# Performance work log

Measured on AMD Instinct MI355X. Metric: run time of the kernel, lower is better.

Reference implementation:

```python
import jax, jax.numpy as jnp
import numpy as np

S, B, D, H, DH, E, F = 2048, 2, 512, 8, 64, 8, 1024
TOPK = 2


def setup_inputs() -> dict:
    key = jax.random.key(0)
    ks = jax.random.split(key, 12)
    rn = lambda k, shp, s=0.02: jax.random.normal(k, shp, jnp.float32) * s
    # RoPE tables (half-split convention): (S, DH)
    pos = jnp.arange(S, dtype=jnp.float32)[:, None]
    inv_freq = 1.0 / (10000.0 ** (jnp.arange(0, DH, 2, dtype=jnp.float32) / DH))
    ang = pos * inv_freq[None, :]                       # (S, DH//2)
    cos = jnp.concatenate([jnp.cos(ang), jnp.cos(ang)], axis=-1)
    sin = jnp.concatenate([jnp.sin(ang), jnp.sin(ang)], axis=-1)
    return {
        "src": jax.random.normal(ks[0], (S, B, D), jnp.float32),
        "cos": cos, "sin": sin,
        "Wq": rn(ks[1], (D, D)), "bq": jnp.zeros((D,), jnp.float32),
        "Wk": rn(ks[2], (D, D)), "bk": jnp.zeros((D,), jnp.float32),
        "Wv": rn(ks[3], (D, D)), "bv": jnp.zeros((D,), jnp.float32),
        "Wo": rn(ks[4], (D, D)), "bo": jnp.zeros((D,), jnp.float32),
        "ln1_g": jnp.ones((D,), jnp.float32), "ln1_b": jnp.zeros((D,), jnp.float32),
        "ln2_g": jnp.ones((D,), jnp.float32), "ln2_b": jnp.zeros((D,), jnp.float32),
        "Wg": rn(ks[5], (D, E)),
        "W1": rn(ks[6], (E, D, F)), "B1": jnp.zeros((E, F), jnp.float32),
        "W2": rn(ks[7], (E, F, D)), "B2": jnp.zeros((E, D), jnp.float32),
    }


def _layernorm(x, g, b, eps=1e-5):
    m = x.mean(-1, keepdims=True)
    v = ((x - m) ** 2).mean(-1, keepdims=True)
    return (x - m) * jax.lax.rsqrt(v + eps) * g + b


def _rotate_half(x):
    x1, x2 = jnp.split(x, 2, axis=-1)
    return jnp.concatenate([-x2, x1], axis=-1)


def _forward(src, cos, sin, Wq, bq, Wk, bk, Wv, bv, Wo, bo,
             ln1_g, ln1_b, ln2_g, ln2_b, Wg, W1, B1, W2, B2):
    # ---- RoPE self-attention ----
    q = (src @ Wq + bq).reshape(S, B, H, DH)
    k = (src @ Wk + bk).reshape(S, B, H, DH)
    v = (src @ Wv + bv).reshape(S, B, H, DH)
    c = cos[:, None, None, :]
    s = sin[:, None, None, :]
    q = q * c + _rotate_half(q) * s
    k = k * c + _rotate_half(k) * s
    scores = jnp.einsum("sbhd,tbhd->bhst", q, k) / jnp.sqrt(jnp.float32(DH))
    attn = jax.nn.softmax(scores, axis=-1)              # (B,H,S,S)
    ctx = jnp.einsum("bhst,tbhd->sbhd", attn, v).reshape(S, B, D)
    attn_out = ctx @ Wo + bo
    x = _layernorm(src + attn_out, ln1_g, ln1_b)
    # ---- MoE feed-forward (top-k softmax gating) ----
    xt = x.reshape(S * B, D)                            # (N, D)
    probs = jax.nn.softmax(xt @ Wg, axis=-1)            # (N, E)
    top_v, top_i = jax.lax.top_k(probs, TOPK)           # (N, TOPK)
    top_v = top_v / top_v.sum(-1, keepdims=True)
    N = S * B
    gates = jnp.zeros((N, E), jnp.float32).at[
        jnp.arange(N)[:, None], top_i].add(top_v)       # (N, E)
    h = jax.nn.relu(jnp.einsum("nd,edf->nef", xt, W1) + B1[None])   # (N,E,F)
    eo = jnp.einsum("nef,efd->ned", h, W2) + B2[None]               # (N,E,D)
    moe_out = jnp.einsum("ne,ned->nd", gates, eo).reshape(S, B, D)
    return _layernorm(x + moe_out, ln2_g, ln2_b)


def reference(src, cos, sin, Wq, bq, Wk, bk, Wv, bv, Wo, bo,
              ln1_g, ln1_b, ln2_g, ln2_b, Wg, W1, B1, W2, B2):
    return _forward(src, cos, sin, Wq, bq, Wk, bk, Wv, bv, Wo, bo,
                    ln1_g, ln1_b, ln2_g, ln2_b, Wg, W1, B1, W2, B2)
```

## Files before the change

### kernel.cpp

```cpp
#include <hip/hip_runtime.h>
#include <math.h>

#define S_  2048
#define B_  2
#define D_  512
#define H_  8
#define DH_ 64
#define E_  8
#define F_  1024
#define N_  4096
#define NPAIR_ 8192

typedef __attribute__((ext_vector_type(4))) float f32x4;
typedef __attribute__((ext_vector_type(8))) short short8;
typedef unsigned short u16;

__device__ __forceinline__ u16 f2bf(float f) {
  unsigned u = __builtin_bit_cast(unsigned, f);
  u += 0x7fffu + ((u >> 16) & 1u);
  return (u16)(u >> 16);
}
__device__ __forceinline__ float bf2f(u16 h) {
  unsigned u = ((unsigned)h) << 16;
  return __builtin_bit_cast(float, u);
}

__global__ __launch_bounds__(256) void src_split(const float* __restrict__ in,
                                                 u16* __restrict__ hi,
                                                 u16* __restrict__ lo) {
  size_t i = ((size_t)blockIdx.x * 256 + threadIdx.x) * 8;
  float f[8];
  *(float4*)&f[0] = *(const float4*)&in[i];
  *(float4*)&f[4] = *(const float4*)&in[i + 4];
  short8 h, l;
#pragma unroll
  for (int j = 0; j < 8; ++j) {
    u16 a = f2bf(f[j]);
    h[j] = (short)a;
    l[j] = (short)f2bf(f[j] - bf2f(a));
  }
  *(short8*)&hi[i] = h;
  *(short8*)&lo[i] = l;
}

__global__ __launch_bounds__(256) void wsplit_t(const float* __restrict__ W,
                                                u16* __restrict__ Whi,
                                                u16* __restrict__ Wlo,
                                                int Nn, int K) {
  __shared__ u16 Th[64][72];
  __shared__ u16 Tl[64][72];
  int kb = blockIdx.y * 64, nb = blockIdx.x * 64;
  int r = threadIdx.x >> 2, c0 = (threadIdx.x & 3) * 16;
  const float* wp = &W[(size_t)(kb + r) * Nn + nb + c0];
#pragma unroll
  for (int c = 0; c < 16; c += 4) {
    float4 t = *(const float4*)&wp[c];
    float f[4] = {t.x, t.y, t.z, t.w};
#pragma unroll
    for (int j = 0; j < 4; ++j) {
      u16 a = f2bf(f[j]);
      Th[r][c0 + c + j] = a;
      Tl[r][c0 + c + j] = f2bf(f[j] - bf2f(a));
    }
  }
  __syncthreads();
  short8 h0, h1, l0, l1;
#pragma unroll
  for (int j = 0; j < 8; ++j) {
    h0[j] = (short)Th[c0 + j][r];     h1[j] = (short)Th[c0 + 8 + j][r];
    l0[j] = (short)Tl[c0 + j][r];     l1[j] = (short)Tl[c0 + 8 + j][r];
  }
  size_t ob = (size_t)(nb + r) * K + kb + c0;
  *(short8*)&Whi[ob] = h0;  *(short8*)&Whi[ob + 8] = h1;
  *(short8*)&Wlo[ob] = l0;  *(short8*)&Wlo[ob + 8] = l1;
}

__global__ __launch_bounds__(256) void wtrans(const float* __restrict__ W,
                                              u16* __restrict__ Wt,
                                              int K, int Nn) {
  size_t eo = (size_t)blockIdx.z * K * Nn;
  __shared__ u16 T[64][72];
  int kb = blockIdx.y * 64, nb = blockIdx.x * 64;
  int r = threadIdx.x >> 2, c0 = (threadIdx.x & 3) * 16;
  const float* wp = &W[eo + (size_t)(kb + r) * Nn + nb + c0];
#pragma unroll
  for (int c = 0; c < 16; c += 4) {
    float4 t = *(const float4*)&wp[c];
    T[r][c0 + c + 0] = f2bf(t.x);
    T[r][c0 + c + 1] = f2bf(t.y);
    T[r][c0 + c + 2] = f2bf(t.z);
    T[r][c0 + c + 3] = f2bf(t.w);
  }
  __syncthreads();
  short8 s0, s1;
#pragma unroll
  for (int j = 0; j < 8; ++j) {
    s0[j] = (short)T[c0 + j][r];
    s1[j] = (short)T[c0 + 8 + j][r];
  }
  *(short8*)&Wt[eo + (size_t)(nb + r) * K + kb + c0] = s0;
  *(short8*)&Wt[eo + (size_t)(nb + r) * K + kb + c0 + 8] = s1;
}

__global__ __launch_bounds__(256) void qkv_mfma(const u16* __restrict__ Ah_g,
                                                const u16* __restrict__ Al_g,
                                                const u16* __restrict__ Bh_g,
                                                const u16* __restrict__ Bl_g,
                                                const float* __restrict__ bq,
                                                const float* __restrict__ bk,
                                                const float* __restrict__ bv,
                                                const float* __restrict__ cosb,
                                                const float* __restrict__ sinb,
                                                u16* __restrict__ qh, u16* __restrict__ ql,
                                                u16* __restrict__ kh, u16* __restrict__ kl,
                                                u16* __restrict__ vb) {
  __shared__ u16 Ah[128][40], Al[128][40], Bh[128][40], Bl[128][40];
  int tid = threadIdx.x;
  int w = tid >> 6, l = tid & 63;
  int wr = w >> 1, wc = w & 1;
  int lg = l >> 4, lx = l & 15;
  int m0 = blockIdx.x * 128, n0 = blockIdx.y * 128;
  int sr = tid >> 1, s16 = (tid & 1) * 16;
  const u16* Aph = Ah_g + (size_t)(m0 + sr) * 512;
  const u16* Apl = Al_g + (size_t)(m0 + sr) * 512;
  const u16* Bph = Bh_g + (size_t)(n0 + sr) * 512;
  const u16* Bpl = Bl_g + (size_t)(n0 + sr) * 512;
  f32x4 acc[4][4];
#pragma unroll
  for (int m = 0; m < 4; ++m)
#pragma unroll
    for (int n = 0; n < 4; ++n) acc[m][n] = (f32x4){0.f, 0.f, 0.f, 0.f};
  short8 ah0 = *(const short8*)&Aph[s16];
  short8 ah1 = *(const short8*)&Aph[s16 + 8];
  short8 al0 = *(const short8*)&Apl[s16];
  short8 al1 = *(const short8*)&Apl[s16 + 8];
  short8 bh0 = *(const short8*)&Bph[s16];
  short8 bh1 = *(const short8*)&Bph[s16 + 8];
  short8 bl0 = *(const short8*)&Bpl[s16];
  short8 bl1 = *(const short8*)&Bpl[s16 + 8];
  for (int k0 = 0; k0 < 512; k0 += 32) {
    __syncthreads();
    *(short8*)&Ah[sr][s16] = ah0; *(short8*)&Ah[sr][s16 + 8] = ah1;
    *(short8*)&Al[sr][s16] = al0; *(short8*)&Al[sr][s16 + 8] = al1;
    *(short8*)&Bh[sr][s16] = bh0; *(short8*)&Bh[sr][s16 + 8] = bh1;
    *(short8*)&Bl[sr][s16] = bl0; *(short8*)&Bl[sr][s16 + 8] = bl1;
    __syncthreads();
    if (k0 + 32 < 512) {
      int ko = k0 + 32 + s16;
      ah0 = *(const short8*)&Aph[ko]; ah1 = *(const short8*)&Aph[ko + 8];
      al0 = *(const short8*)&Apl[ko]; al1 = *(const short8*)&Apl[ko + 8];
      bh0 = *(const short8*)&Bph[ko]; bh1 = *(const short8*)&Bph[ko + 8];
      bl0 = *(const short8*)&Bpl[ko]; bl1 = *(const short8*)&Bpl[ko + 8];
    }
    short8 fah[4], fal[4], fbh[4], fbl[4];
#pragma unroll
    for (int m = 0; m < 4; ++m) {
      fah[m] = *(const short8*)&Ah[wr * 64 + m * 16 + lx][lg * 8];
      fal[m] = *(const short8*)&Al[wr * 64 + m * 16 + lx][lg * 8];
    }
#pragma unroll
    for (int n = 0; n < 4; ++n) {
      fbh[n] = *(const short8*)&Bh[wc * 64 + n * 16 + lx][lg * 8];
      fbl[n] = *(const short8*)&Bl[wc * 64 + n * 16 + lx][lg * 8];
    }
#pragma unroll
    for (int m = 0; m < 4; ++m)
#pragma unroll
      for (int n = 0; n < 4; ++n) {
        acc[m][n] = __builtin_amdgcn_mfma_f32_16x16x32_bf16(fah[m], fbh[n], acc[m][n], 0, 0, 0);
        acc[m][n] = __builtin_amdgcn_mfma_f32_16x16x32_bf16(fal[m], fbh[n], acc[m][n], 0, 0, 0);
        acc[m][n] = __builtin_amdgcn_mfma_f32_16x16x32_bf16(fah[m], fbl[n], acc[m][n], 0, 0, 0);
      }
  }
  int tcolbase = n0 + wc * 64;
  int tsel = tcolbase >> 9;
  int hbase = tcolbase & 511;
  const float* bias = (tsel == 0) ? bq : (tsel == 1) ? bk : bv;
  if (tsel == 2) {
#pragma unroll
    for (int m = 0; m < 4; ++m)
#pragma unroll
      for (int i = 0; i < 4; ++i) {
        int row = m0 + wr * 64 + m * 16 + lg * 4 + i;
#pragma unroll
        for (int n = 0; n < 4; ++n) {
          int col = hbase + n * 16 + lx;
          vb[(size_t)row * 512 + col] = f2bf(acc[m][n][i] + bias[col]);
        }
      }
  } else {
    u16* oh = tsel ? kh : qh;
    u16* ol = tsel ? kl : ql;
    float qsc = tsel ? 1.f : 0.125f;
#pragma unroll
    for (int m = 0; m < 4; ++m)
#pragma unroll
      for (int i = 0; i < 4; ++i) {
        int row = m0 + wr * 64 + m * 16 + lg * 4 + i;
        int s = row >> 1;
#pragma unroll
        for (int n = 0; n < 2; ++n) {
          int dln = n * 16 + lx;
          float c  = cosb[s * 64 + dln];
          float sn = sinb[s * 64 + dln];
          float a  = acc[m][n][i]     + bias[hbase + dln];
          float b2 = acc[m][n + 2][i] + bias[hbase + dln + 32];
          float ra = (a * c - b2 * sn) * qsc;
          float rb = (b2 * c + a * sn) * qsc;
          size_t ix = (size_t)row * 512 + hbase + dln;
          u16 rah = f2bf(ra);
          oh[ix] = rah; ol[ix] = f2bf(ra - bf2f(rah));
          u16 rbh = f2bf(rb);
          oh[ix + 32] = rbh; ol[ix + 32] = f2bf(rb - bf2f(rbh));
        }
      }
  }
}

__global__ __launch_bounds__(256) void attn_mfma2(const u16* __restrict__ qh,
                                                  const u16* __restrict__ ql,
                                                  const u16* __restrict__ kh,
                                                  const u16* __restrict__ kl,
                                                  const u16* __restrict__ vbuf,
                                                  u16* __restrict__ poh,
                                                  u16* __restrict__ pol,
                                                  float* __restrict__ pml) {
  __shared__ u16 Khi[64][72];
  __shared__ u16 Klo[64][72];
  __shared__ u16 Vt[64][72];
  __shared__ u16 Pl[4][16][72];
  int tid = threadIdx.x;
  int w = tid >> 6, l = tid & 63;
  int lg = l >> 4, lx = l & 15;
  int f = blockIdx.x;
  int xcd = f & 7, j = f >> 3;
  int slab = xcd + 8 * (j & 3);
  int qt = j >> 2;
  int bh = slab >> 1, kvh = slab & 1;
  int b = bh >> 3, h = bh & 7;

  short8 qfh[2], qfl[2];
  {
    int qrow = qt * 64 + w * 16 + lx;
    size_t qo = (size_t)(qrow * 2 + b) * 512 + h * 64 + lg * 8;
    qfh[0] = *(const short8*)&qh[qo];
    qfh[1] = *(const short8*)&qh[qo + 32];
    qfl[0] = *(const short8*)&ql[qo];
    qfl[1] = *(const short8*)&ql[qo + 32];
  }

  f32x4 o_acc[4];
#pragma unroll
  for (int dg = 0; dg < 4; ++dg) o_acc[dg] = (f32x4){0.f, 0.f, 0.f, 0.f};
  float m_run[4], l_run[4];
#pragma unroll
  for (int i = 0; i < 4; ++i) { m_run[i] = -1e30f; l_run[i] = 0.f; }

  int kvr = tid >> 2, ds4 = (tid & 3) * 16;
  int kvc = tid & 63, dsg = (tid >> 6) * 16;
  int psw = ((lx >> 2) & 3) << 3;

  short8 rkh0, rkh1, rkl0, rkl1, rv0, rv1;
  {
    int t0 = kvh * 1024;
    size_t ko = (size_t)((t0 + kvr) * 2 + b) * 512 + h * 64 + ds4;
    rkh0 = *(const short8*)&kh[ko]; rkh1 = *(const short8*)&kh[ko + 8];
    rkl0 = *(const short8*)&kl[ko]; rkl1 = *(const short8*)&kl[ko + 8];
    size_t vo = (size_t)((t0 + kvc) * 2 + b) * 512 + h * 64 + dsg;
    rv0 = *(const short8*)&vbuf[vo]; rv1 = *(const short8*)&vbuf[vo + 8];
  }

  for (int tt = 0; tt < 1024; tt += 64) {
    __syncthreads();
    *(short8*)&Khi[kvr][ds4]     = rkh0;
    *(short8*)&Khi[kvr][ds4 + 8] = rkh1;
    *(short8*)&Klo[kvr][ds4]     = rkl0;
    *(short8*)&Klo[kvr][ds4 + 8] = rkl1;
#pragma unroll
    for (int c = 0; c < 8; ++c) {
      Vt[dsg + c][kvc] = (u16)rv0[c];
      Vt[dsg + 8 + c][kvc] = (u16)rv1[c];
    }
    __syncthreads();
    if (tt + 64 < 1024) {
      int t0 = kvh * 1024 + tt + 64;
      size_t ko = (size_t)((t0 + kvr) * 2 + b) * 512 + h * 64 + ds4;
      rkh0 = *(const short8*)&kh[ko]; rkh1 = *(const short8*)&kh[ko + 8];
      rkl0 = *(const short8*)&kl[ko]; rkl1 = *(const short8*)&kl[ko + 8];
      size_t vo = (size_t)((t0 + kvc) * 2 + b) * 512 + h * 64 + dsg;
      rv0 = *(const short8*)&vbuf[vo]; rv1 = *(const short8*)&vbuf[vo + 8];
    }

    f32x4 sc[4];
#pragma unroll
    for (int cg = 0; cg < 4; ++cg) {
      short8 kf0 = *(const short8*)&Khi[cg * 16 + lx][lg * 8];
      short8 kf1 = *(const short8*)&Khi[cg * 16 + lx][32 + lg * 8];
      short8 kg0 = *(const short8*)&Klo[cg * 16 + lx][lg * 8];
      short8 kg1 = *(const short8*)&Klo[cg * 16 + lx][32 + lg * 8];
      f32x4 a = (f32x4){0.f, 0.f, 0.f, 0.f};
      a = __builtin_amdgcn_mfma_f32_16x16x32_bf16(qfh[0], kf0, a, 0, 0, 0);
      a = __builtin_amdgcn_mfma_f32_16x16x32_bf16(qfh[1], kf1, a, 0, 0, 0);
      a = __builtin_amdgcn_mfma_f32_16x16x32_bf16(qfl[0], kf0, a, 0, 0, 0);
      a = __builtin_amdgcn_mfma_f32_16x16x32_bf16(qfl[1], kf1, a, 0, 0, 0);
      a = __builtin_amdgcn_mfma_f32_16x16x32_bf16(qfh[0], kg0, a, 0, 0, 0);
      a = __builtin_amdgcn_mfma_f32_16x16x32_bf16(qfh[1], kg1, a, 0, 0, 0);
      sc[cg] = a;
    }

#pragma unroll
    for (int i = 0; i < 4; ++i) {
      float s0 = sc[0][i], s1 = sc[1][i], s2 = sc[2][i], s3 = sc[3][i];
      float tm = fmaxf(fmaxf(s0, s1), fmaxf(s2, s3));
      tm = fmaxf(tm, __shfl_xor(tm, 1));
      tm = fmaxf(tm, __shfl_xor(tm, 2));
      tm = fmaxf(tm, __shfl_xor(tm, 4));
      tm = fmaxf(tm, __shfl_xor(tm, 8));
      float mn = fmaxf(m_run[i], tm);
      float corr = __expf(m_run[i] - mn);
      m_run[i] = mn;
      float p0 = __expf(s0 - mn), p1 = __expf(s1 - mn);
      float p2 = __expf(s2 - mn), p3 = __expf(s3 - mn);
      float ts = p0 + p1 + p2 + p3;
      ts += __shfl_xor(ts, 1); ts += __shfl_xor(ts, 2);
      ts += __shfl_xor(ts, 4); ts += __shfl_xor(ts, 8);
      l_run[i] = l_run[i] * corr + ts;
#pragma unroll
      for (int dg = 0; dg < 4; ++dg) o_acc[dg][i] *= corr;
      int row = lg * 4 + i;
      int sw = ((row >> 2) & 3) << 3;
      Pl[w][row][lx ^ sw]        = f2bf(p0);
      Pl[w][row][(16 + lx) ^ sw] = f2bf(p1);
      Pl[w][row][(32 + lx) ^ sw] = f2bf(p2);
      Pl[w][row][(48 + lx) ^ sw] = f2bf(p3);
    }

    short8 pa0 = *(const short8*)&Pl[w][lx][(lg * 8) ^ psw];
    short8 pa1 = *(const short8*)&Pl[w][lx][(32 + lg * 8) ^ psw];
#pragma unroll
    for (int dg = 0; dg < 4; ++dg) {
      short8 v0 = *(const short8*)&Vt[dg * 16 + lx][lg * 8];
      short8 v1 = *(const short8*)&Vt[dg * 16 + lx][32 + lg * 8];
      o_acc[dg] = __builtin_amdgcn_mfma_f32_16x16x32_bf16(pa0, v0, o_acc[dg], 0, 0, 0);
      o_acc[dg] = __builtin_amdgcn_mfma_f32_16x16x32_bf16(pa1, v1, o_acc[dg], 0, 0, 0);
    }
  }

#pragma unroll
  for (int i = 0; i < 4; ++i) {
    int srow = qt * 64 + w * 16 + lg * 4 + i;
    int row2 = srow * 2 + b;
    size_t base = (size_t)kvh * ((size_t)N_ * D_) + (size_t)row2 * 512 + h * 64;
#pragma unroll
    for (int dg = 0; dg < 4; ++dg) {
      float val = o_acc[dg][i];
      u16 hi = f2bf(val);
      poh[base + dg * 16 + lx] = hi;
      pol[base + dg * 16 + lx] = f2bf(val - bf2f(hi));
    }
    if (lx == 0) {
      int u = row2 * 8 + h;
      pml[(size_t)kvh * 65536 + u * 2 + 0] = m_run[i];
      pml[(size_t)kvh * 65536 + u * 2 + 1] = l_run[i];
    }
  }
}

__global__ __launch_bounds__(256) void merge_attn2(const u16* __restrict__ poh,
                                                   const u16* __restrict__ pol,
                                                   const float* __restrict__ pml,
                                                   u16* __restrict__ ch,
                                                   u16* __restrict__ cl) {
  int u = blockIdx.x * 4 + (threadIdx.x >> 6);
  int lane = threadIdx.x & 63;
  float m0 = pml[u * 2], l0 = pml[u * 2 + 1];
  float m1 = pml[65536 + u * 2], l1 = pml[65536 + u * 2 + 1];
  float m = fmaxf(m0, m1);
  float e0 = __expf(m0 - m), e1 = __expf(m1 - m);
  float inv = 1.f / (l0 * e0 + l1 * e1);
  int n = u >> 3, h = u & 7;
  size_t base = (size_t)n * 512 + h * 64 + lane;
  const size_t PO1 = (size_t)N_ * D_;
  float v0 = bf2f(poh[base]) + bf2f(pol[base]);
  float v1 = bf2f(poh[PO1 + base]) + bf2f(pol[PO1 + base]);
  float val = (v0 * e0 + v1 * e1) * inv;
  u16 hi = f2bf(val);
  ch[base] = hi;
  cl[base] = f2bf(val - bf2f(hi));
}

__global__ __launch_bounds__(256) void wo_mfma(const u16* __restrict__ Ah_g,
                                               const u16* __restrict__ Al_g,
                                               const u16* __restrict__ Bh_g,
                                               const u16* __restrict__ Bl_g,
                                               const float* __restrict__ bias,
                                               float* __restrict__ C) {
  __shared__ u16 Ah[128][40], Al[128][40], Bh[128][40], Bl[128][40];
  int tid = threadIdx.x;
  int w = tid >> 6, l = tid & 63;
  int wr = w >> 1, wc = w & 1;
  int lg = l >> 4, lx = l & 15;
  int m0 = blockIdx.x * 128, n0 = blockIdx.y * 128;
  int sr = tid >> 1, s16 = (tid & 1) * 16;
  const u16* Aph = Ah_g + (size_t)(m0 + sr) * 512;
  const u16* Apl = Al_g + (size_t)(m0 + sr) * 512;
  const u16* Bph = Bh_g + (size_t)(n0 + sr) * 512;
  const u16* Bpl = Bl_g + (size_t)(n0 + sr) * 512;
  f32x4 acc[4][4];
#pragma unroll
  for (int m = 0; m < 4; ++m)
#pragma unroll
    for (int n = 0; n < 4; ++n) acc[m][n] = (f32x4){0.f, 0.f, 0.f, 0.f};
  short8 ah0 = *(const short8*)&Aph[s16];
  short8 ah1 = *(const short8*)&Aph[s16 + 8];
  short8 al0 = *(const short8*)&Apl[s16];
  short8 al1 = *(const short8*)&Apl[s16 + 8];
  short8 bh0 = *(const short8*)&Bph[s16];
  short8 bh1 = *(const short8*)&Bph[s16 + 8];
  short8 bl0 = *(const short8*)&Bpl[s16];
  short8 bl1 = *(const short8*)&Bpl[s16 + 8];
  for (int k0 = 0; k0 < 512; k0 += 32) {
    __syncthreads();
    *(short8*)&Ah[sr][s16] = ah0; *(short8*)&Ah[sr][s16 + 8] = ah1;
    *(short8*)&Al[sr][s16] = al0; *(short8*)&Al[sr][s16 + 8] = al1;
    *(short8*)&Bh[sr][s16] = bh0; *(short8*)&Bh[sr][s16 + 8] = bh1;
    *(short8*)&Bl[sr][s16] = bl0; *(short8*)&Bl[sr][s16 + 8] = bl1;
    __syncthreads();
    if (k0 + 32 < 512) {
      int ko = k0 + 32 + s16;
      ah0 = *(const short8*)&Aph[ko]; ah1 = *(const short8*)&Aph[ko + 8];
      al0 = *(const short8*)&Apl[ko]; al1 = *(const short8*)&Apl[ko + 8];
      bh0 = *(const short8*)&Bph[ko]; bh1 = *(const short8*)&Bph[ko + 8];
      bl0 = *(const short8*)&Bpl[ko]; bl1 = *(const short8*)&Bpl[ko + 8];
    }
    short8 fah[4], fal[4], fbh[4], fbl[4];
#pragma unroll
    for (int m = 0; m < 4; ++m) {
      fah[m] = *(const short8*)&Ah[wr * 64 + m * 16 + lx][lg * 8];
      fal[m] = *(const short8*)&Al[wr * 64 + m * 16 + lx][lg * 8];
    }
#pragma unroll
    for (int n = 0; n < 4; ++n) {
      fbh[n] = *(const short8*)&Bh[wc * 64 + n * 16 + lx][lg * 8];
      fbl[n] = *(const short8*)&Bl[wc * 64 + n * 16 + lx][lg * 8];
    }
#pragma unroll
    for (int m = 0; m < 4; ++m)
#pragma unroll
      for (int n = 0; n < 4; ++n) {
        acc[m][n] = __builtin_amdgcn_mfma_f32_16x16x32_bf16(fah[m], fbh[n], acc[m][n], 0, 0, 0);
        acc[m][n] = __builtin_amdgcn_mfma_f32_16x16x32_bf16(fal[m], fbh[n], acc[m][n], 0, 0, 0);
        acc[m][n] = __builtin_amdgcn_mfma_f32_16x16x32_bf16(fah[m], fbl[n], acc[m][n], 0, 0, 0);
      }
  }
#pragma unroll
  for (int m = 0; m < 4; ++m)
#pragma unroll
    for (int i = 0; i < 4; ++i) {
      int row = m0 + wr * 64 + m * 16 + lg * 4 + i;
#pragma unroll
      for (int n = 0; n < 4; ++n) {
        int col = n0 + wc * 64 + n * 16 + lx;
        C[(size_t)row * 512 + col] = acc[m][n][i] + bias[col];
      }
    }
}

__global__ __launch_bounds__(256) void ln_res(const float* __restrict__ a,
                                              const float* __restrict__ b,
                                              const float* __restrict__ g,
                                              const float* __restrict__ beta,
                                              float* __restrict__ out,
                                              u16* __restrict__ obf) {
  int n = blockIdx.x * 4 + (threadIdx.x >> 6);
  int lane = threadIdx.x & 63;
  float v[8];
  float s = 0.f;
#pragma unroll
  for (int i = 0; i < 8; ++i) {
    int d = lane + 64 * i;
    v[i] = a[(size_t)n * D_ + d] + b[(size_t)n * D_ + d];
    s += v[i];
  }
#pragma unroll
  for (int m = 32; m; m >>= 1) s += __shfl_xor(s, m);
  float mean = s * (1.f / D_);
  float s2 = 0.f;
#pragma unroll
  for (int i = 0; i < 8; ++i) { float t = v[i] - mean; s2 += t * t; }
#pragma unroll
  for (int m = 32; m; m >>= 1) s2 += __shfl_xor(s2, m);
  float r = rsqrtf(s2 * (1.f / D_) + 1e-5f);
#pragma unroll
  for (int i = 0; i < 8; ++i) {
    int d = lane + 64 * i;
    float val = (v[i] - mean) * r * g[d] + beta[d];
    out[(size_t)n * D_ + d] = val;
    obf[(size_t)n * D_ + d] = f2bf(val);
  }
}

__global__ __launch_bounds__(256) void ln2_final(const float* __restrict__ x,
                                                 const u16* __restrict__ mp,
                                                 const float* __restrict__ g,
                                                 const float* __restrict__ beta,
                                                 float* __restrict__ out) {
  int n = blockIdx.x * 4 + (threadIdx.x >> 6);
  int lane = threadIdx.x & 63;
  float v[8];
  float s = 0.f;
#pragma unroll
  for (int i = 0; i < 8; ++i) {
    int d = lane + 64 * i;
    v[i] = x[(size_t)n * D_ + d] + bf2f(mp[(size_t)(2 * n) * D_ + d]) +
           bf2f(mp[(size_t)(2 * n + 1) * D_ + d]);
    s += v[i];
  }
#pragma unroll
  for (int m = 32; m; m >>= 1) s += __shfl_xor(s, m);
  float mean = s * (1.f / D_);
  float s2 = 0.f;
#pragma unroll
  for (int i = 0; i < 8; ++i) { float t = v[i] - mean; s2 += t * t; }
#pragma unroll
  for (int m = 32; m; m >>= 1) s2 += __shfl_xor(s2, m);
  float r = rsqrtf(s2 * (1.f / D_) + 1e-5f);
#pragma unroll
  for (int i = 0; i < 8; ++i) {
    int d = lane + 64 * i;
    out[(size_t)n * D_ + d] = (v[i] - mean) * r * g[d] + beta[d];
  }
}

__global__ __launch_bounds__(256) void gate_compute(const float* __restrict__ x,
                                                    const float* __restrict__ Wg,
                                                    float* __restrict__ gp,
                                                    int* __restrict__ tope) {
  int n = blockIdx.x * 4 + (threadIdx.x >> 6);
  int lane = threadIdx.x & 63;
  float p[E_] = {};
  for (int d = lane; d < D_; d += 64) {
    float xv = x[(size_t)n * D_ + d];
    const float* wr = &Wg[(size_t)d * E_];
#pragma unroll
    for (int e = 0; e < E_; ++e) p[e] += xv * wr[e];
  }
#pragma unroll
  for (int e = 0; e < E_; ++e)
#pragma unroll
    for (int m = 32; m; m >>= 1) p[e] += __shfl_xor(p[e], m);
  if (lane == 0) {
    float mx = p[0];
#pragma unroll
    for (int e = 1; e < E_; ++e) mx = fmaxf(mx, p[e]);
    float q[E_];
#pragma unroll
    for (int e = 0; e < E_; ++e) q[e] = expf(p[e] - mx);
    int e1 = 0;
#pragma unroll
    for (int e = 1; e < E_; ++e) if (q[e] > q[e1]) e1 = e;
    int e2 = (e1 == 0) ? 1 : 0;
#pragma unroll
    for (int e = 0; e < E_; ++e) if (e != e1 && q[e] > q[e2]) e2 = e;
    float denom = q[e1] + q[e2];
    gp[n * 2] = q[e1] / denom;
    gp[n * 2 + 1] = q[e2] / denom;
    tope[n] = e1 | (e2 << 8);
  }
}

__global__ __launch_bounds__(256) void route_build(const int* __restrict__ tope,
                                                   int* __restrict__ cnt,
                                                   int* __restrict__ lst) {
  int e = blockIdx.x;
  __shared__ int wsum[4];
  __shared__ int basem;
  int tid = threadIdx.x;
  int w = tid >> 6, lane = tid & 63;
  if (tid == 0) basem = 0;
  __syncthreads();
  for (int c0 = 0; c0 < N_; c0 += 256) {
    int n = c0 + tid;
    int te = tope[n];
    int e1 = te & 0xff, e2 = (te >> 8) & 0xff;
    bool m2 = (e2 == e);
    bool flag = (e1 == e) || m2;
    unsigned long long mask = __ballot(flag);
    int wpre = __popcll(mask & ((1ull << lane) - 1ull));
    if (lane == 0) wsum[w] = __popcll(mask);
    __syncthreads();
    int woff = 0;
    for (int i = 0; i < w; ++i) woff += wsum[i];
    int total = wsum[0] + wsum[1] + wsum[2] + wsum[3];
    if (flag) lst[e * N_ + basem + woff + wpre] = n * 2 + (m2 ? 1 : 0);
    __syncthreads();
    if (tid == 0) basem += total;
    __syncthreads();
  }
  if (tid == 0) cnt[e] = basem;
}

template <int MODE>
__global__ __launch_bounds__(256) void moe_mfma(const u16* __restrict__ Abase,
                                                const u16* __restrict__ Wt,
                                                const float* __restrict__ bias,
                                                const float* __restrict__ gp,
                                                u16* __restrict__ outp,
                                                const int* __restrict__ cnt,
                                                const int* __restrict__ lst) {
  constexpr int K  = MODE ? 1024 : 512;
  constexpr int Nn = MODE ? 512 : 1024;
  constexpr int NT = Nn / 128;
  constexpr int NI = K / 32;
  int fidx = blockIdx.x;
  int e = fidx & 7;
  int r = fidx >> 3;
  int nt = r % NT;
  int mt = r / NT;
  int c = cnt[e];
  int m0 = mt * 64;
  if (m0 >= c) return;
  int off = 0;
#pragma unroll
  for (int i = 0; i < E_; ++i) if (i < e) off += cnt[i];
  int n0 = nt * 128;
  __shared__ u16 As[64][40];
  __shared__ u16 Bs[128][40];
  int tid = threadIdx.x;
  int w = tid >> 6, l = tid & 63;
  int lg = l >> 4, lx = l & 15;
  int arow = tid >> 2, aseg = (tid & 3) * 8;
  int brow = tid >> 1, bseg = (tid & 1) * 16;
  int ar = m0 + arow; if (ar >= c) ar = c - 1;
  const u16* Ap;
  if (MODE == 0) Ap = Abase + (size_t)(lst[e * N_ + ar] >> 1) * 512 + aseg;
  else           Ap = Abase + (size_t)(off + ar) * 1024 + aseg;
  const u16* Bp = Wt + (size_t)e * K * Nn + (size_t)(n0 + brow) * K + bseg;

  f32x4 acc[4][2];
#pragma unroll
  for (int m = 0; m < 4; ++m)
#pragma unroll
    for (int n = 0; n < 2; ++n) acc[m][n] = (f32x4){0.f, 0.f, 0.f, 0.f};

  short8 pa  = *(const short8*)&Ap[0];
  short8 pb0 = *(const short8*)&Bp[0];
  short8 pb1 = *(const short8*)&Bp[8];
  for (int kk = 0; kk < NI; ++kk) {
    __syncthreads();
    *(short8*)&As[arow][aseg] = pa;
    *(short8*)&Bs[brow][bseg] = pb0;
    *(short8*)&Bs[brow][bseg + 8] = pb1;
    __syncthreads();
    if (kk + 1 < NI) {
      int ko = (kk + 1) * 32;
      pa  = *(const short8*)&Ap[ko];
      pb0 = *(const short8*)&Bp[ko];
      pb1 = *(const short8*)&Bp[ko + 8];
    }
    short8 af[4], bf[2];
#pragma unroll
    for (int m = 0; m < 4; ++m)
      af[m] = *(const short8*)&As[m * 16 + lx][lg * 8];
#pragma unroll
    for (int n = 0; n < 2; ++n)
      bf[n] = *(const short8*)&Bs[w * 32 + n * 16 + lx][lg * 8];
#pragma unroll
    for (int m = 0; m < 4; ++m)
#pragma unroll
      for (int n = 0; n < 2; ++n)
        acc[m][n] = __builtin_amdgcn_mfma_f32_16x16x32_bf16(af[m], bf[n], acc[m][n], 0, 0, 0);
  }
#pragma unroll
  for (int m = 0; m < 4; ++m)
#pragma unroll
    for (int i = 0; i < 4; ++i) {
      int rr = m0 + m * 16 + lg * 4 + i;
      if (rr < c) {
#pragma unroll
        for (int n = 0; n < 2; ++n) {
          int col = n0 + w * 32 + n * 16 + lx;
          float val = acc[m][n][i] + bias[e * Nn + col];
          if (MODE == 0) {
            outp[(size_t)(off + rr) * 1024 + col] = f2bf(fmaxf(val, 0.f));
          } else {
            int p = lst[e * N_ + rr];
            outp[(size_t)p * 512 + col] = f2bf(gp[p] * val);
          }
        }
      }
    }
}

extern "C" void kernel_launch(void* const* d_in, const int* in_sizes, int n_in,
                              void* d_out, int out_size, void* d_ws, size_t ws_size,
                              hipStream_t stream) {
  const float* src  = (const float*)d_in[0];
  const float* cosb = (const float*)d_in[1];
  const float* sinb = (const float*)d_in[2];
  const float* Wq   = (const float*)d_in[3];
  const float* bq   = (const float*)d_in[4];
  const float* Wk   = (const float*)d_in[5];
  const float* bk   = (const float*)d_in[6];
  const float* Wv   = (const float*)d_in[7];
  const float* bv   = (const float*)d_in[8];
  const float* Wo   = (const float*)d_in[9];
  const float* bo   = (const float*)d_in[10];
  const float* ln1g = (const float*)d_in[11];
  const float* ln1b = (const float*)d_in[12];
  const float* ln2g = (const float*)d_in[13];
  const float* ln2b = (const float*)d_in[14];
  const float* Wg   = (const float*)d_in[15];
  const float* W1   = (const float*)d_in[16];
  const float* B1   = (const float*)d_in[17];
  const float* W2   = (const float*)d_in[18];
  const float* B2   = (const float*)d_in[19];
  float* out = (float*)d_out;
  char* wsb = (char*)d_ws;

  const size_t MB1 = 1u << 20;
  u16* sh   = (u16*)(wsb + 0 * MB1);
  u16* sl   = (u16*)(wsb + 4 * MB1);
  u16* qhb  = (u16*)(wsb + 8 * MB1);
  u16* qlb  = (u16*)(wsb + 12 * MB1);
  u16* khb  = (u16*)(wsb + 16 * MB1);
  u16* klb  = (u16*)(wsb + 20 * MB1);
  u16* vbuf = (u16*)(wsb + 24 * MB1);
  u16* poh  = (u16*)(wsb + 28 * MB1);
  u16* pol  = (u16*)(wsb + 36 * MB1);
  float* pml = (float*)(wsb + 44 * MB1);
  float* aob = (float*)(wsb + 28 * MB1);
  float* xb  = (float*)(wsb + 36 * MB1);
  u16* xbf   = (u16*)(wsb + 44 * MB1);
  u16* Wqkv_hi = (u16*)(wsb + 48 * MB1);
  u16* Wqkv_lo = (u16*)(wsb + 48 * MB1 + 1572864);
  u16* Wo_hi   = (u16*)(wsb + 48 * MB1 + 3145728);
  u16* Wo_lo   = (u16*)(wsb + 48 * MB1 + 3670016);
  u16* W1t     = (u16*)(wsb + 52 * MB1);
  u16* W2t     = (u16*)(wsb + 28 * MB1);
  float* gpb   = (float*)(wsb + 60 * MB1);
  int* cnt     = (int*)(wsb + 60 * MB1 + 32768);
  int* lst     = (int*)(wsb + 60 * MB1 + 32768 + 64);
  int* tope    = (int*)(wsb + 60 * MB1 + 32768 + 64 + 131072);
  u16* ch  = sh;
  u16* cl  = sl;
  u16* hbf = (u16*)(wsb + 8 * MB1);
  u16* mp  = (u16*)(wsb + 0 * MB1);

  dim3 blk(256);
  src_split<<<dim3(1024), blk, 0, stream>>>(src, sh, sl);
  wsplit_t<<<dim3(8, 8), blk, 0, stream>>>(Wq, Wqkv_hi, Wqkv_lo, 512, 512);
  wsplit_t<<<dim3(8, 8), blk, 0, stream>>>(Wk, Wqkv_hi + 512 * 512, Wqkv_lo + 512 * 512, 512, 512);
  wsplit_t<<<dim3(8, 8), blk, 0, stream>>>(Wv, Wqkv_hi + 1024 * 512, Wqkv_lo + 1024 * 512, 512, 512);
  wsplit_t<<<dim3(8, 8), blk, 0, stream>>>(Wo, Wo_hi, Wo_lo, 512, 512);
  qkv_mfma<<<dim3(32, 12), blk, 0, stream>>>(sh, sl, Wqkv_hi, Wqkv_lo, bq, bk, bv,
                                             cosb, sinb, qhb, qlb, khb, klb, vbuf);
  attn_mfma2<<<dim3(1024), blk, 0, stream>>>(qhb, qlb, khb, klb, vbuf, poh, pol, pml);
  merge_attn2<<<dim3(8192), blk, 0, stream>>>(poh, pol, pml, ch, cl);
  wo_mfma<<<dim3(32, 4), blk, 0, stream>>>(ch, cl, Wo_hi, Wo_lo, bo, aob);
  ln_res<<<dim3(1024), blk, 0, stream>>>(src, aob, ln1g, ln1b, xb, xbf);
  wtrans<<<dim3(8, 16, 8), blk, 0, stream>>>(W2, W2t, 1024, 512);
  wtrans<<<dim3(16, 8, 8), blk, 0, stream>>>(W1, W1t, 512, 1024);
  gate_compute<<<dim3(1024), blk, 0, stream>>>(xb, Wg, gpb, tope);
  route_build<<<dim3(8), blk, 0, stream>>>(tope, cnt, lst);
  moe_mfma<0><<<dim3(8 * 8 * 64), blk, 0, stream>>>(xbf, W1t, B1, gpb, hbf, cnt, lst);
  moe_mfma<1><<<dim3(8 * 4 * 64), blk, 0, stream>>>(hbf, W2t, B2, gpb, mp, cnt, lst);
  ln2_final<<<dim3(1024), blk, 0, stream>>>(xb, mp, ln2g, ln2b, out);
}
```

Measured before the change: 251.1 us.

## Transpose attention MFMA operands so each lane owns one query row's scores

Swaps the A/B operands of the QK^T and PV MFMAs so the score tile comes out transposed, with each lane holding scores for a single query row. Softmax max and sum then run over 16 in-register values plus two cross-lane shuffles, instead of four separate 16-lane shuffle reductions per row. The row statistics become scalars rather than per-row arrays. P is packed into 32-bit dwords in a new swizzled LDS layout for the PV MFMA, and output stores become per-lane rows with a different write pattern. This cuts shuffle and exp bookkeeping per tile, at the cost of a new LDS layout and possibly less coalesced output stores.

```diff
diff --git a/kernel.cpp b/kernel.cpp
--- a/kernel.cpp
+++ b/kernel.cpp
@@ -228,7 +228,7 @@
   __shared__ u16 Khi[64][72];
   __shared__ u16 Klo[64][72];
   __shared__ u16 Vt[64][72];
-  __shared__ u16 Pl[4][16][72];
+  __shared__ unsigned P2[4][16][32];
   int tid = threadIdx.x;
   int w = tid >> 6, l = tid & 63;
   int lg = l >> 4, lx = l & 15;
@@ -252,13 +252,11 @@
   f32x4 o_acc[4];
 #pragma unroll
   for (int dg = 0; dg < 4; ++dg) o_acc[dg] = (f32x4){0.f, 0.f, 0.f, 0.f};
-  float m_run[4], l_run[4];
-#pragma unroll
-  for (int i = 0; i < 4; ++i) { m_run[i] = -1e30f; l_run[i] = 0.f; }
+  float m_run = -1e30f, l_run = 0.f;
 
   int kvr = tid >> 2, ds4 = (tid & 3) * 16;
   int kvc = tid & 63, dsg = (tid >> 6) * 16;
-  int psw = ((lx >> 2) & 3) << 3;
+  int psw = (lx & 7) << 2;
 
   short8 rkh0, rkh1, rkl0, rkl1, rv0, rv1;
   {
@@ -299,69 +297,78 @@
       short8 kg0 = *(const short8*)&Klo[cg * 16 + lx][lg * 8];
       short8 kg1 = *(const short8*)&Klo[cg * 16 + lx][32 + lg * 8];
       f32x4 a = (f32x4){0.f, 0.f, 0.f, 0.f};
-      a = __builtin_amdgcn_mfma_f32_16x16x32_bf16(qfh[0], kf0, a, 0, 0, 0);
-      a = __builtin_amdgcn_mfma_f32_16x16x32_bf16(qfh[1], kf1, a, 0, 0, 0);
-      a = __builtin_amdgcn_mfma_f32_16x16x32_bf16(qfl[0], kf0, a, 0, 0, 0);
-      a = __builtin_amdgcn_mfma_f32_16x16x32_bf16(qfl[1], kf1, a, 0, 0, 0);
-      a = __builtin_amdgcn_mfma_f32_16x16x32_bf16(qfh[0], kg0, a, 0, 0, 0);
-      a = __builtin_amdgcn_mfma_f32_16x16x32_bf16(qfh[1], kg1, a, 0, 0, 0);
+      a = __builtin_amdgcn_mfma_f32_16x16x32_bf16(kf0, qfh[0], a, 0, 0, 0);
+      a = __builtin_amdgcn_mfma_f32_16x16x32_bf16(kf1, qfh[1], a, 0, 0, 0);
+      a = __builtin_amdgcn_mfma_f32_16x16x32_bf16(kf0, qfl[0], a, 0, 0, 0);
+      a = __builtin_amdgcn_mfma_f32_16x16x32_bf16(kf1, qfl[1], a, 0, 0, 0);
+      a = __builtin_amdgcn_mfma_f32_16x16x32_bf16(kg0, qfh[0], a, 0, 0, 0);
+      a = __builtin_amdgcn_mfma_f32_16x16x32_bf16(kg1, qfh[1], a, 0, 0, 0);
       sc[cg] = a;
     }
 
-#pragma unroll
-    for (int i = 0; i < 4; ++i) {
-      float s0 = sc[0][i], s1 = sc[1][i], s2 = sc[2][i], s3 = sc[3][i];
-      float tm = fmaxf(fmaxf(s0, s1), fmaxf(s2, s3));
-      tm = fmaxf(tm, __shfl_xor(tm, 1));
-      tm = fmaxf(tm, __shfl_xor(tm, 2));
-      tm = fmaxf(tm, __shfl_xor(tm, 4));
-      tm = fmaxf(tm, __shfl_xor(tm, 8));
-      float mn = fmaxf(m_run[i], tm);
-      float corr = __expf(m_run[i] - mn);
-      m_run[i] = mn;
-      float p0 = __expf(s0 - mn), p1 = __expf(s1 - mn);
-      float p2 = __expf(s2 - mn), p3 = __expf(s3 - mn);
-      float ts = p0 + p1 + p2 + p3;
-      ts += __shfl_xor(ts, 1); ts += __shfl_xor(ts, 2);
-      ts += __shfl_xor(ts, 4); ts += __shfl_xor(ts, 8);
-      l_run[i] = l_run[i] * corr + ts;
-#pragma unroll
-      for (int dg = 0; dg < 4; ++dg) o_acc[dg][i] *= corr;
-      int row = lg * 4 + i;
-      int sw = ((row >> 2) & 3) << 3;
-      Pl[w][row][lx ^ sw]        = f2bf(p0);
-      Pl[w][row][(16 + lx) ^ sw] = f2bf(p1);
-      Pl[w][row][(32 + lx) ^ sw] = f2bf(p2);
-      Pl[w][row][(48 + lx) ^ sw] = f2bf(p3);
-    }
-
-    short8 pa0 = *(const short8*)&Pl[w][lx][(lg * 8) ^ psw];
-    short8 pa1 = *(const short8*)&Pl[w][lx][(32 + lg * 8) ^ psw];
+    float tm = sc[0][0];
+#pragma unroll
+    for (int cg = 0; cg < 4; ++cg)
+#pragma unroll
+      for (int i = 0; i < 4; ++i) tm = fmaxf(tm, sc[cg][i]);
+    tm = fmaxf(tm, __shfl_xor(tm, 16));
+    tm = fmaxf(tm, __shfl_xor(tm, 32));
+    float mn = fmaxf(m_run, tm);
+    float corr = __expf(m_run - mn);
+    m_run = mn;
+    float ts = 0.f;
+#pragma unroll
+    for (int cg = 0; cg < 4; ++cg)
+#pragma unroll
+      for (int i = 0; i < 4; ++i) {
+        float pv = __expf(sc[cg][i] - mn);
+        sc[cg][i] = pv;
+        ts += pv;
+      }
+    ts += __shfl_xor(ts, 16);
+    ts += __shfl_xor(ts, 32);
+    l_run = l_run * corr + ts;
+#pragma unroll
+    for (int dg = 0; dg < 4; ++dg) o_acc[dg] *= corr;
+
+#pragma unroll
+    for (int cg = 0; cg < 4; ++cg)
+#pragma unroll
+      for (int t = 0; t < 2; ++t) {
+        unsigned dw = (unsigned)f2bf(sc[cg][2 * t]) |
+                      ((unsigned)f2bf(sc[cg][2 * t + 1]) << 16);
+        P2[w][lx][(8 * cg + 2 * lg + t) ^ psw] = dw;
+      }
+    short8 pf0 = *(const short8*)&P2[w][lx][(4 * lg) ^ psw];
+    short8 pf1 = *(const short8*)&P2[w][lx][(16 + 4 * lg) ^ psw];
+
 #pragma unroll
     for (int dg = 0; dg < 4; ++dg) {
       short8 v0 = *(const short8*)&Vt[dg * 16 + lx][lg * 8];
       short8 v1 = *(const short8*)&Vt[dg * 16 + lx][32 + lg * 8];
-      o_acc[dg] = __builtin_amdgcn_mfma_f32_16x16x32_bf16(pa0, v0, o_acc[dg], 0, 0, 0);
-      o_acc[dg] = __builtin_amdgcn_mfma_f32_16x16x32_bf16(pa1, v1, o_acc[dg], 0, 0, 0);
-    }
-  }
-
-#pragma unroll
-  for (int i = 0; i < 4; ++i) {
-    int srow = qt * 64 + w * 16 + lg * 4 + i;
-    int row2 = srow * 2 + b;
+      o_acc[dg] = __builtin_amdgcn_mfma_f32_16x16x32_bf16(v0, pf0, o_acc[dg], 0, 0, 0);
+      o_acc[dg] = __builtin_amdgcn_mfma_f32_16x16x32_bf16(v1, pf1, o_acc[dg], 0, 0, 0);
+    }
+  }
+
+  {
+    int qrow = qt * 64 + w * 16 + lx;
+    int row2 = qrow * 2 + b;
     size_t base = (size_t)kvh * ((size_t)N_ * D_) + (size_t)row2 * 512 + h * 64;
 #pragma unroll
-    for (int dg = 0; dg < 4; ++dg) {
-      float val = o_acc[dg][i];
-      u16 hi = f2bf(val);
-      poh[base + dg * 16 + lx] = hi;
-      pol[base + dg * 16 + lx] = f2bf(val - bf2f(hi));
-    }
-    if (lx == 0) {
+    for (int dg = 0; dg < 4; ++dg)
+#pragma unroll
+      for (int i = 0; i < 4; ++i) {
+        int d = dg * 16 + 4 * lg + i;
+        float val = o_acc[dg][i];
+        u16 hi = f2bf(val);
+        poh[base + d] = hi;
+        pol[base + d] = f2bf(val - bf2f(hi));
+      }
+    if (lg == 0) {
       int u = row2 * 8 + h;
-      pml[(size_t)kvh * 65536 + u * 2 + 0] = m_run[i];
-      pml[(size_t)kvh * 65536 + u * 2 + 1] = l_run[i];
+      pml[(size_t)kvh * 65536 + u * 2 + 0] = m_run;
+      pml[(size_t)kvh * 65536 + u * 2 + 1] = l_run;
     }
   }
 }
```

Measured after the change: 237.8 us. 1.06x faster.
